# Optimization experiments

Measured on AMD Instinct MI355X. Metric: run time of the kernel, lower is better.

## Reference

```python
import jax
import jax.numpy as jnp
import numpy as np
from jax import lax

IOU_THRESH = 0.5
TOP, LEFT, BOTTOM, RIGHT = 0, 1, 2, 3


def setup_inputs() -> dict:
    key = jax.random.key(0)
    k1, k2, k3, k4, k5 = jax.random.split(key, 5)
    B, N, C = 4, 3000, 21
    # plausible boxes in (top, left, bottom, right) with positive height/width
    tl = jax.random.uniform(k1, (B, N, 2), dtype=jnp.float32) * 800.0
    wh = jax.random.uniform(k2, (B, N, 2), dtype=jnp.float32) * 200.0 + 1.0
    nms_reg = jnp.concatenate([tl, tl + wh], axis=2)
    nms_cls = jax.random.normal(k3, (B, N, 1), dtype=jnp.float32)
    rcnn_reg = jax.random.normal(k4, (B, N, 4), dtype=jnp.float32) * 2.0
    rcnn_cls = jax.random.normal(k5, (B, N, C), dtype=jnp.float32)
    return {"nms_reg": nms_reg, "nms_cls": nms_cls,
            "rcnn_reg": rcnn_reg, "rcnn_cls": rcnn_cls, "reduction": 16}


def _pairwise_iou(boxes):
    # boxes: [N, 4] in (top, left, bottom, right). IoU is invariant to the
    # (x, y) axis permutation the original applies before torchvision.nms.
    t, l, b, r = boxes[:, 0], boxes[:, 1], boxes[:, 2], boxes[:, 3]
    area = jnp.maximum(b - t, 0.0) * jnp.maximum(r - l, 0.0)  # [N]
    ih = jnp.maximum(jnp.minimum(b[:, None], b[None, :]) - jnp.maximum(t[:, None], t[None, :]), 0.0)
    iw = jnp.maximum(jnp.minimum(r[:, None], r[None, :]) - jnp.maximum(l[:, None], l[None, :]), 0.0)
    inter = ih * iw  # [N, N]
    union = area[:, None] + area[None, :] - inter
    return inter / jnp.maximum(union, 1e-9)


def _nms_keep(iou, scores):
    # Greedy NMS over one class. iou: [N, N]; scores: [N] (-inf = not this class).
    # Matches torchvision.ops.nms: suppress boxes with IoU > threshold.
    N = scores.shape[0]
    idx = jnp.arange(N)

    def step(state, _):
        rem, keep = state
        i = jnp.argmax(rem)
        valid = rem[i] > -jnp.inf
        keep = keep.at[i].set(valid)
        suppress = (iou[i] > IOU_THRESH) | (idx == i)
        rem = jnp.where(valid & suppress, -jnp.inf, rem)
        return (rem, keep), None

    (_, keep), _ = lax.scan(step, (scores, jnp.zeros(N, dtype=bool)), None, length=N)
    return keep


def reference(nms_reg, nms_cls, rcnn_reg, rcnn_cls, reduction):
    red = jnp.float32(reduction)
    # round top/left down, bottom/right up on the feature grid, back to pixels
    nms_reg_rounded = jnp.concatenate(
        [jnp.floor(nms_reg[:, :, :2] * red), jnp.ceil(nms_reg[:, :, 2:] * red)],
        axis=2) / red
    # rcnn_reg[:, :, c] += nms_reg_rounded[:, :, c] for all 4 coords
    boxes = rcnn_reg + nms_reg_rounded  # [B, N, 4]
    probs = jax.nn.softmax(rcnn_cls, axis=2)  # [B, N, C]
    nms_cls_sig = jax.nn.sigmoid(nms_cls)

    amax = jnp.argmax(probs, axis=2)  # [B, N]
    C = probs.shape[2]
    class_ids = jnp.arange(1, C)  # skip background class 0
    # per-class masked scores: [B, C-1, N]
    cls_scores = jnp.transpose(probs, (0, 2, 1))[:, 1:, :]
    scores = jnp.where(amax[:, None, :] == class_ids[None, :, None],
                       cls_scores, -jnp.inf)

    iou = jax.vmap(_pairwise_iou)(boxes)  # [B, N, N] (shared across classes)
    keep_per_class = jax.vmap(lambda io, sc: jax.vmap(lambda s: _nms_keep(io, s))(sc))(iou, scores)  # [B, C-1, N]
    keep = jnp.any(keep_per_class, axis=1)  # [B, N]; argmax classes are disjoint

    return (nms_reg_rounded, nms_cls_sig, boxes, probs, keep)
```

## Files before the change

kernel.cpp:

```cpp
#include <hip/hip_runtime.h>
#include <cfloat>
#include <climits>

#define B 4
#define N 3000
#define C 21
#define SORT_N 256
#define WORDS 4
#define NMS_BLOCKS (B * (C - 1))
#define PW_BLOCKS 12
#define TPB 1024


__device__ __forceinline__ int softmax_am(const float* __restrict__ lg,
                                          float* __restrict__ pmax_out,
                                          float* __restrict__ pstore) {
    float m = lg[0];
    #pragma unroll
    for (int c = 1; c < C; ++c) m = fmaxf(m, lg[c]);
    float p[C];
    float sum = 0.0f;
    #pragma unroll
    for (int c = 0; c < C; ++c) {
        p[c] = expf(__fsub_rn(lg[c], m));
        sum = __fadd_rn(sum, p[c]);
    }
    float best = -1.0f; int bc = 0;
    #pragma unroll
    for (int c = 0; c < C; ++c) {
        float pc = __fdiv_rn(p[c], sum);
        if (pstore) pstore[c] = pc;
        if (pc > best) { best = pc; bc = c; }
    }
    *pmax_out = best;
    return bc;
}

__device__ __forceinline__ void make_boxes(float4 nr, float4 rr, float red,
                                           float4* rounded, float4* box) {
    float r0 = floorf(__fmul_rn(nr.x, red)) / red;
    float r1 = floorf(__fmul_rn(nr.y, red)) / red;
    float r2 = ceilf (__fmul_rn(nr.z, red)) / red;
    float r3 = ceilf (__fmul_rn(nr.w, red)) / red;
    *rounded = make_float4(r0, r1, r2, r3);
    *box = make_float4(__fadd_rn(rr.x, r0), __fadd_rn(rr.y, r1),
                       __fadd_rn(rr.z, r2), __fadd_rn(rr.w, r3));
}

__global__ __launch_bounds__(TPB) void fused_kernel(
    const float* __restrict__ nms_reg,
    const float* __restrict__ nms_cls,
    const float* __restrict__ rcnn_reg,
    const float* __restrict__ rcnn_cls,
    const int* __restrict__ red_p,
    float* __restrict__ out)
{
    const int tid = threadIdx.x;

    float* out_round = out;
    float* out_sig   = out + B * N * 4;
    float* out_boxes = out + B * N * 5;
    float* out_probs = out + B * N * 9;
    float* out_keep  = out + B * N * 30;

    if (blockIdx.x >= NMS_BLOCKS) {
        const int bn = (blockIdx.x - NMS_BLOCKS) * TPB + tid;
        if (bn >= B * N) return;

        float red = (float)(*red_p);

        float4 nr = ((const float4*)nms_reg)[bn];
        float4 rr = ((const float4*)rcnn_reg)[bn];
        float4 rounded, box;
        make_boxes(nr, rr, red, &rounded, &box);
        ((float4*)out_round)[bn] = rounded;
        ((float4*)out_boxes)[bn] = box;

        float x = nms_cls[bn];
        float s;
        if (x >= 0.0f) s = 1.0f / (1.0f + expf(-x));
        else { float e = expf(x); s = e / (1.0f + e); }
        out_sig[bn] = s;

        float pm;
        int am = softmax_am(rcnn_cls + (size_t)bn * C, &pm, out_probs + (size_t)bn * C);

        if (am == 0) out_keep[bn] = 0.0f;
        return;
    }

    const int b = blockIdx.x / (C - 1);
    const int c = blockIdx.x % (C - 1) + 1;
    const int lane = tid & 63;

    __shared__ int   gid[SORT_N];
    __shared__ float gsc[SORT_N];
    __shared__ int   rnk[SORT_N];
    __shared__ int   sid[SORT_N];
    __shared__ float bt[SORT_N], bl[SORT_N], bb[SORT_N], br_[SORT_N], ar[SORT_N];
    __shared__ __align__(16) unsigned long long msk[SORT_N][WORDS];
    __shared__ int mcount;

    if (tid == 0) mcount = 0;
    if (tid < SORT_N) rnk[tid] = 0;
    __syncthreads();

    #pragma unroll
    for (int chunk = 0; chunk < 3; ++chunk) {
        int n = chunk * TPB + tid;
        bool match = false;
        float pm = 0.0f;
        if (n < N) {
            int am = softmax_am(rcnn_cls + (size_t)(b * N + n) * C, &pm, nullptr);
            match = (am == c);
        }
        unsigned long long mb = __ballot(match);
        int base = 0;
        if (lane == 0 && mb) base = atomicAdd(&mcount, __popcll(mb));
        base = __shfl(base, 0);
        if (match) {
            int pos = base + __popcll(mb & ((1ull << lane) - 1ull));
            if (pos < SORT_N) { gid[pos] = n; gsc[pos] = pm; }
        }
    }
    __syncthreads();
    const int M = min(mcount, SORT_N);

    {
        int e = tid & 255, q = tid >> 8;
        if (e < M) {
            float mys = gsc[e]; int myi = gid[e];
            int j0 = q * 64, j1 = min(j0 + 64, M);
            int partial = 0;
            for (int j = j0; j < j1; ++j) {
                float sj = gsc[j]; int ij = gid[j];
                partial += ((sj > mys) || (sj == mys && ij < myi)) ? 1 : 0;
            }
            if (partial) atomicAdd(&rnk[e], partial);
        }
    }
    __syncthreads();

    if (tid < M) {
        float red = (float)(*red_p);
        int n = gid[tid];
        int rank = rnk[tid];
        float4 nr = ((const float4*)nms_reg)[b * N + n];
        float4 rr = ((const float4*)rcnn_reg)[b * N + n];
        float4 rounded, box;
        make_boxes(nr, rr, red, &rounded, &box);
        sid[rank] = n;
        bt[rank] = box.x; bl[rank] = box.y; bb[rank] = box.z; br_[rank] = box.w;
        ar[rank] = __fmul_rn(fmaxf(__fsub_rn(box.z, box.x), 0.0f),
                             fmaxf(__fsub_rn(box.w, box.y), 0.0f));
    }
    __syncthreads();

    {
        int g = tid >> 8;
        int j = tid & 255;
        int w = (tid >> 6) & 3;
        float jt = 0.f, jl = 0.f, jb = 0.f, jr = 0.f, ja = 0.f;
        if (j < M) { jt = bt[j]; jl = bl[j]; jb = bb[j]; jr = br_[j]; ja = ar[j]; }
        int r0 = g * 64, r1 = min(r0 + 64, M);
        for (int r = r0; r < r1; ++r) {
            float rt = bt[r], rl = bl[r], rb = bb[r], rr = br_[r], ra = ar[r];
            bool supp = false;
            if (j > r && j < M) {
                float ih = fmaxf(__fsub_rn(fminf(rb, jb), fmaxf(rt, jt)), 0.0f);
                float iw = fmaxf(__fsub_rn(fminf(rr, jr), fmaxf(rl, jl)), 0.0f);
                float inter = __fmul_rn(ih, iw);
                float uni = __fsub_rn(__fadd_rn(ra, ja), inter);
                float iou = __fdiv_rn(inter, fmaxf(uni, 1e-9f));
                supp = iou > 0.5f;
            }
            unsigned long long wm = __ballot(supp);
            if (lane == 0) msk[r][w] = wm;
        }
    }
    __syncthreads();

    auto onesk = [](int k) -> unsigned long long {
        return k <= 0 ? 0ull : (k >= 64 ? ~0ull : ((1ull << k) - 1ull));
    };
    unsigned long long a0 = onesk(M), a1 = onesk(M - 64), a2 = onesk(M - 128), a3 = onesk(M - 192);

    {
        int e = min(64, M);
        #pragma unroll 4
        for (int i = 0; i < e; ++i) {
            unsigned long long sel = 0ull - ((a0 >> i) & 1ull);
            a0 &= ~(msk[i][0] & sel);
            a1 &= ~(msk[i][1] & sel);
            a2 &= ~(msk[i][2] & sel);
            a3 &= ~(msk[i][3] & sel);
        }
    }
    {
        int e = min(128, M);
        #pragma unroll 4
        for (int i = 64; i < e; ++i) {
            unsigned long long sel = 0ull - ((a1 >> (i - 64)) & 1ull);
            a1 &= ~(msk[i][1] & sel);
            a2 &= ~(msk[i][2] & sel);
            a3 &= ~(msk[i][3] & sel);
        }
    }
    {
        int e = min(192, M);
        #pragma unroll 4
        for (int i = 128; i < e; ++i) {
            unsigned long long sel = 0ull - ((a2 >> (i - 128)) & 1ull);
            a2 &= ~(msk[i][2] & sel);
            a3 &= ~(msk[i][3] & sel);
        }
    }
    {
        int e = min(256, M);
        #pragma unroll 4
        for (int i = 192; i < e; ++i) {
            unsigned long long sel = 0ull - ((a3 >> (i - 192)) & 1ull);
            a3 &= ~(msk[i][3] & sel);
        }
    }

    if (tid < M) {
        unsigned long long aw = (tid < 64) ? a0 : (tid < 128) ? a1 : (tid < 192) ? a2 : a3;
        bool kept = (aw >> (tid & 63)) & 1ull;
        int n = sid[tid];
        out_keep[b * N + n] = (kept && n != 0) ? 1.0f : 0.0f;
    }
}

extern "C" void kernel_launch(void* const* d_in, const int* in_sizes, int n_in,
                              void* d_out, int out_size, void* d_ws, size_t ws_size,
                              hipStream_t stream) {
    const float* nms_reg  = (const float*)d_in[0];
    const float* nms_cls  = (const float*)d_in[1];
    const float* rcnn_reg = (const float*)d_in[2];
    const float* rcnn_cls = (const float*)d_in[3];
    const int*   red_p    = (const int*)d_in[4];
    float* out = (float*)d_out;

    dim3 grid(NMS_BLOCKS + PW_BLOCKS);
    fused_kernel<<<grid, TPB, 0, stream>>>(nms_reg, nms_cls, rcnn_reg, rcnn_cls, red_p, out);
}
```

Baseline: 111.7 us.

## Compute softmax argmax once and share it with NMS blocks via flags

```diff
diff --git a/kernel.cpp b/kernel.cpp
--- a/kernel.cpp
+++ b/kernel.cpp
@@ -7,34 +7,11 @@
 #define C 21
 #define SORT_N 256
 #define WORDS 4
+#define PW_BLOCKS 12
 #define NMS_BLOCKS (B * (C - 1))
-#define PW_BLOCKS 12
 #define TPB 1024
-
-
-__device__ __forceinline__ int softmax_am(const float* __restrict__ lg,
-                                          float* __restrict__ pmax_out,
-                                          float* __restrict__ pstore) {
-    float m = lg[0];
-    #pragma unroll
-    for (int c = 1; c < C; ++c) m = fmaxf(m, lg[c]);
-    float p[C];
-    float sum = 0.0f;
-    #pragma unroll
-    for (int c = 0; c < C; ++c) {
-        p[c] = expf(__fsub_rn(lg[c], m));
-        sum = __fadd_rn(sum, p[c]);
-    }
-    float best = -1.0f; int bc = 0;
-    #pragma unroll
-    for (int c = 0; c < C; ++c) {
-        float pc = __fdiv_rn(p[c], sum);
-        if (pstore) pstore[c] = pc;
-        if (pc > best) { best = pc; bc = c; }
-    }
-    *pmax_out = best;
-    return bc;
-}
+#define FLAG_MAGIC 0x5A5A5A5A
+
 
 __device__ __forceinline__ void make_boxes(float4 nr, float4 rr, float red,
                                            float4* rounded, float4* box) {
@@ -53,7 +30,9 @@
     const float* __restrict__ rcnn_reg,
     const float* __restrict__ rcnn_cls,
     const int* __restrict__ red_p,
-    float* __restrict__ out)
+    float* __restrict__ out,
+    int* __restrict__ flags,
+    unsigned long long* __restrict__ cw)
 {
     const int tid = threadIdx.x;
 
@@ -63,34 +42,58 @@
     float* out_probs = out + B * N * 9;
     float* out_keep  = out + B * N * 30;
 
-    if (blockIdx.x >= NMS_BLOCKS) {
-        const int bn = (blockIdx.x - NMS_BLOCKS) * TPB + tid;
-        if (bn >= B * N) return;
-
-        float red = (float)(*red_p);
-
-        float4 nr = ((const float4*)nms_reg)[bn];
-        float4 rr = ((const float4*)rcnn_reg)[bn];
-        float4 rounded, box;
-        make_boxes(nr, rr, red, &rounded, &box);
-        ((float4*)out_round)[bn] = rounded;
-        ((float4*)out_boxes)[bn] = box;
-
-        float x = nms_cls[bn];
-        float s;
-        if (x >= 0.0f) s = 1.0f / (1.0f + expf(-x));
-        else { float e = expf(x); s = e / (1.0f + e); }
-        out_sig[bn] = s;
-
-        float pm;
-        int am = softmax_am(rcnn_cls + (size_t)bn * C, &pm, out_probs + (size_t)bn * C);
-
-        if (am == 0) out_keep[bn] = 0.0f;
+    if (blockIdx.x < PW_BLOCKS) {
+        const int bn = blockIdx.x * TPB + tid;
+        if (bn < B * N) {
+            float red = (float)(*red_p);
+
+            float4 nr = ((const float4*)nms_reg)[bn];
+            float4 rr = ((const float4*)rcnn_reg)[bn];
+            float4 rounded, box;
+            make_boxes(nr, rr, red, &rounded, &box);
+            ((float4*)out_round)[bn] = rounded;
+            ((float4*)out_boxes)[bn] = box;
+
+            float x = nms_cls[bn];
+            float s;
+            if (x >= 0.0f) s = 1.0f / (1.0f + expf(-x));
+            else { float e = expf(x); s = e / (1.0f + e); }
+            out_sig[bn] = s;
+
+            const float* lg = rcnn_cls + (size_t)bn * C;
+            float m = lg[0];
+            #pragma unroll
+            for (int c = 1; c < C; ++c) m = fmaxf(m, lg[c]);
+            float p[C];
+            float sum = 0.0f;
+            #pragma unroll
+            for (int c = 0; c < C; ++c) {
+                p[c] = expf(__fsub_rn(lg[c], m));
+                sum = __fadd_rn(sum, p[c]);
+            }
+            float* po = out_probs + (size_t)bn * C;
+            float best = -1.0f; int am = 0;
+            #pragma unroll
+            for (int c = 0; c < C; ++c) {
+                float pc = __fdiv_rn(p[c], sum);
+                po[c] = pc;
+                if (pc > best) { best = pc; am = c; }
+            }
+            cw[bn] = ((unsigned long long)__float_as_uint(best) << 32) | (unsigned int)am;
+            if (am == 0) out_keep[bn] = 0.0f;
+        }
+        __syncthreads();
+        if (tid == 0) {
+            __threadfence();
+            __hip_atomic_store(&flags[blockIdx.x], FLAG_MAGIC,
+                               __ATOMIC_RELEASE, __HIP_MEMORY_SCOPE_AGENT);
+        }
         return;
     }
 
-    const int b = blockIdx.x / (C - 1);
-    const int c = blockIdx.x % (C - 1) + 1;
+    const int nid = blockIdx.x - PW_BLOCKS;
+    const int b = nid / (C - 1);
+    const int c = nid % (C - 1) + 1;
     const int lane = tid & 63;
 
     __shared__ int   gid[SORT_N];
@@ -99,9 +102,16 @@
     __shared__ int   sid[SORT_N];
     __shared__ float bt[SORT_N], bl[SORT_N], bb[SORT_N], br_[SORT_N], ar[SORT_N];
     __shared__ __align__(16) unsigned long long msk[SORT_N][WORDS];
+    __shared__ unsigned long long aout[WORDS];
     __shared__ int mcount;
 
-    if (tid == 0) mcount = 0;
+    if (tid == 0) {
+        mcount = 0;
+        for (int i = 0; i < PW_BLOCKS; ++i)
+            while (__hip_atomic_load(&flags[i], __ATOMIC_ACQUIRE,
+                                     __HIP_MEMORY_SCOPE_AGENT) != FLAG_MAGIC)
+                __builtin_amdgcn_s_sleep(1);
+    }
     if (tid < SORT_N) rnk[tid] = 0;
     __syncthreads();
 
@@ -111,8 +121,12 @@
         bool match = false;
         float pm = 0.0f;
         if (n < N) {
-            int am = softmax_am(rcnn_cls + (size_t)(b * N + n) * C, &pm, nullptr);
-            match = (am == c);
+            unsigned long long v = __hip_atomic_load(&cw[b * N + n], __ATOMIC_RELAXED,
+                                                     __HIP_MEMORY_SCOPE_AGENT);
+            if ((int)(v & 0xffffffffull) == c) {
+                match = true;
+                pm = __uint_as_float((unsigned int)(v >> 32));
+            }
         }
         unsigned long long mb = __ballot(match);
         int base = 0;
@@ -163,16 +177,17 @@
         float jt = 0.f, jl = 0.f, jb = 0.f, jr = 0.f, ja = 0.f;
         if (j < M) { jt = bt[j]; jl = bl[j]; jb = bb[j]; jr = br_[j]; ja = ar[j]; }
         int r0 = g * 64, r1 = min(r0 + 64, M);
+        const double THR = 0.5 + 0x1p-25;
         for (int r = r0; r < r1; ++r) {
-            float rt = bt[r], rl = bl[r], rb = bb[r], rr = br_[r], ra = ar[r];
+            float rt = bt[r], rl = bl[r], rb = bb[r], rr2 = br_[r], ra = ar[r];
             bool supp = false;
             if (j > r && j < M) {
                 float ih = fmaxf(__fsub_rn(fminf(rb, jb), fmaxf(rt, jt)), 0.0f);
-                float iw = fmaxf(__fsub_rn(fminf(rr, jr), fmaxf(rl, jl)), 0.0f);
+                float iw = fmaxf(__fsub_rn(fminf(rr2, jr), fmaxf(rl, jl)), 0.0f);
                 float inter = __fmul_rn(ih, iw);
                 float uni = __fsub_rn(__fadd_rn(ra, ja), inter);
-                float iou = __fdiv_rn(inter, fmaxf(uni, 1e-9f));
-                supp = iou > 0.5f;
+                float den = fmaxf(uni, 1e-9f);
+                supp = ((double)inter > (double)den * THR);
             }
             unsigned long long wm = __ballot(supp);
             if (lane == 0) msk[r][w] = wm;
@@ -180,52 +195,55 @@
     }
     __syncthreads();
 
-    auto onesk = [](int k) -> unsigned long long {
-        return k <= 0 ? 0ull : (k >= 64 ? ~0ull : ((1ull << k) - 1ull));
-    };
-    unsigned long long a0 = onesk(M), a1 = onesk(M - 64), a2 = onesk(M - 128), a3 = onesk(M - 192);
-
-    {
-        int e = min(64, M);
-        #pragma unroll 4
-        for (int i = 0; i < e; ++i) {
-            unsigned long long sel = 0ull - ((a0 >> i) & 1ull);
-            a0 &= ~(msk[i][0] & sel);
-            a1 &= ~(msk[i][1] & sel);
-            a2 &= ~(msk[i][2] & sel);
-            a3 &= ~(msk[i][3] & sel);
-        }
-    }
-    {
-        int e = min(128, M);
-        #pragma unroll 4
-        for (int i = 64; i < e; ++i) {
-            unsigned long long sel = 0ull - ((a1 >> (i - 64)) & 1ull);
-            a1 &= ~(msk[i][1] & sel);
-            a2 &= ~(msk[i][2] & sel);
-            a3 &= ~(msk[i][3] & sel);
-        }
-    }
-    {
-        int e = min(192, M);
-        #pragma unroll 4
-        for (int i = 128; i < e; ++i) {
-            unsigned long long sel = 0ull - ((a2 >> (i - 128)) & 1ull);
-            a2 &= ~(msk[i][2] & sel);
-            a3 &= ~(msk[i][3] & sel);
-        }
-    }
-    {
-        int e = min(256, M);
-        #pragma unroll 4
-        for (int i = 192; i < e; ++i) {
-            unsigned long long sel = 0ull - ((a3 >> (i - 192)) & 1ull);
-            a3 &= ~(msk[i][3] & sel);
-        }
-    }
+    if (tid < 64) {
+        auto onesk = [](int k) -> unsigned long long {
+            return k <= 0 ? 0ull : (k >= 64 ? ~0ull : ((1ull << k) - 1ull));
+        };
+        unsigned long long a0 = onesk(M), a1 = onesk(M - 64), a2 = onesk(M - 128), a3 = onesk(M - 192);
+        {
+            int e = min(64, M);
+            #pragma unroll 4
+            for (int i = 0; i < e; ++i) {
+                unsigned long long sel = 0ull - ((a0 >> i) & 1ull);
+                a0 &= ~(msk[i][0] & sel);
+                a1 &= ~(msk[i][1] & sel);
+                a2 &= ~(msk[i][2] & sel);
+                a3 &= ~(msk[i][3] & sel);
+            }
+        }
+        {
+            int e = min(128, M);
+            #pragma unroll 4
+            for (int i = 64; i < e; ++i) {
+                unsigned long long sel = 0ull - ((a1 >> (i - 64)) & 1ull);
+                a1 &= ~(msk[i][1] & sel);
+                a2 &= ~(msk[i][2] & sel);
+                a3 &= ~(msk[i][3] & sel);
+            }
+        }
+        {
+            int e = min(192, M);
+            #pragma unroll 4
+            for (int i = 128; i < e; ++i) {
+                unsigned long long sel = 0ull - ((a2 >> (i - 128)) & 1ull);
+                a2 &= ~(msk[i][2] & sel);
+                a3 &= ~(msk[i][3] & sel);
+            }
+        }
+        {
+            int e = min(256, M);
+            #pragma unroll 4
+            for (int i = 192; i < e; ++i) {
+                unsigned long long sel = 0ull - ((a3 >> (i - 192)) & 1ull);
+                a3 &= ~(msk[i][3] & sel);
+            }
+        }
+        if (lane == 0) { aout[0] = a0; aout[1] = a1; aout[2] = a2; aout[3] = a3; }
+    }
+    __syncthreads();
 
     if (tid < M) {
-        unsigned long long aw = (tid < 64) ? a0 : (tid < 128) ? a1 : (tid < 192) ? a2 : a3;
+        unsigned long long aw = aout[tid >> 6];
         bool kept = (aw >> (tid & 63)) & 1ull;
         int n = sid[tid];
         out_keep[b * N + n] = (kept && n != 0) ? 1.0f : 0.0f;
@@ -241,7 +259,10 @@
     const float* rcnn_cls = (const float*)d_in[3];
     const int*   red_p    = (const int*)d_in[4];
     float* out = (float*)d_out;
-
-    dim3 grid(NMS_BLOCKS + PW_BLOCKS);
-    fused_kernel<<<grid, TPB, 0, stream>>>(nms_reg, nms_cls, rcnn_reg, rcnn_cls, red_p, out);
+    int* flags = (int*)d_ws;
+    unsigned long long* cw = (unsigned long long*)((char*)d_ws + 256);
+
+    dim3 grid(PW_BLOCKS + NMS_BLOCKS);
+    fused_kernel<<<grid, TPB, 0, stream>>>(nms_reg, nms_cls, rcnn_reg, rcnn_cls,
+                                           red_p, out, flags, cw);
 }
```

Result: slower. 114.9 us (+2.9%).
